# Kernel optimization log

Hardware: AMD Instinct MI355X
Metric: run time of the kernel (lower is better)

The kernel has to match this reference:

```python
import jax, jax.numpy as jnp
import numpy as np
from jax import lax

B, N, F_IN, F_OUT = 64, 256, 768, 256


def setup_inputs() -> dict:
    key = jax.random.key(0)
    ks = jax.random.split(key, 14)
    s = 0.02
    h = jax.random.normal(ks[0], (B, N, F_IN), jnp.float32)
    adj = jax.random.randint(ks[1], (B, N, N), 0, 2).astype(jnp.float32)
    return {
        'h': h,
        'adj': adj,
        'emb_W': jax.random.normal(ks[2], (F_OUT, F_IN), jnp.float32) * s,
        'ioux_W': jax.random.normal(ks[3], (2 * F_OUT, F_OUT), jnp.float32) * s,
        'ioux_b': jax.random.normal(ks[4], (2 * F_OUT,), jnp.float32) * s,
        'iouh_W': jax.random.normal(ks[5], (2 * F_OUT, F_OUT), jnp.float32) * s,
        'iouh_b': jax.random.normal(ks[6], (2 * F_OUT,), jnp.float32) * s,
        'coux_W': jax.random.normal(ks[7], (F_OUT, F_OUT), jnp.float32) * s,
        'coux_b': jax.random.normal(ks[8], (F_OUT,), jnp.float32) * s,
        'couh_W': jax.random.normal(ks[9], (F_OUT, F_OUT), jnp.float32) * s,
        'couh_b': jax.random.normal(ks[10], (F_OUT,), jnp.float32) * s,
        'fc_W': jax.random.normal(ks[11], (2, F_OUT), jnp.float32) * s,
        'fc_b': jax.random.normal(ks[12], (2,), jnp.float32) * s,
    }


def reference(h, adj, emb_W, ioux_W, ioux_b, iouh_W, iouh_b,
              coux_W, coux_b, couh_W, couh_b, fc_W, fc_b):
    # h: [B,N,F_IN], adj: [B,N,N]
    h_e = jnp.einsum('bnf,of->bno', h, emb_W)            # emb(h), no bias
    d = jnp.sum(adj, axis=-1)                            # row-degree [B,N]
    d_inv = jnp.where(d != 0, 1.0 / jnp.where(d != 0, d, 1.0), 0.0)
    # x-side projections depend only on the original h_e -> precompute once
    iou_x = jnp.einsum('bnf,of->bno', h_e, ioux_W) + ioux_b   # [B,N,2F]
    cou_x = jnp.einsum('bnf,of->bno', h_e, coux_W) + coux_b   # [B,N,F]

    n_nodes = h.shape[1]

    def step(h_copy, i):
        # Tree_Parent_AGG row i: p[b,i] = d_inv[b,i] * sum_j adj[b,j,i] * h_copy[b,j]
        adj_col = lax.dynamic_index_in_dim(adj, i, axis=2, keepdims=False)   # [B,N]
        dinv_i = lax.dynamic_index_in_dim(d_inv, i, axis=1, keepdims=False)  # [B]
        x_parent = jnp.einsum('bn,bnd->bd', adj_col, h_copy) * dinv_i[:, None]
        iou = lax.dynamic_index_in_dim(iou_x, i, axis=1, keepdims=False) \
              + x_parent @ iouh_W.T + iouh_b
        r, z = jnp.split(iou, 2, axis=1)
        r = jax.nn.sigmoid(r)
        z = jax.nn.sigmoid(z)
        hc = jnp.tanh(lax.dynamic_index_in_dim(cou_x, i, axis=1, keepdims=False)
                      + (r * x_parent) @ couh_W.T + couh_b)
        h_new = z * x_parent + (1.0 - z) * hc
        h_copy = lax.dynamic_update_index_in_dim(h_copy, h_new, i, axis=1)
        return h_copy, None

    h_final, _ = lax.scan(step, h_e, jnp.arange(n_nodes))
    pooled = jnp.max(h_final, axis=1)                    # [B,F]
    return pooled @ fc_W.T + fc_b                        # [B,2]
```

## Files before the change

kernel.cpp:

```cpp
#include <hip/hip_runtime.h>
#include <hip/hip_fp16.h>

#define NB    64
#define NN    256
#define FIN   768
#define FOUT  256

typedef _Float16 half8v __attribute__((ext_vector_type(8)));
typedef float    float4v __attribute__((ext_vector_type(4)));

__device__ inline unsigned char enc8(float v){
#if __has_builtin(__builtin_amdgcn_cvt_pk_fp8_f32)
  return (unsigned char)(__builtin_amdgcn_cvt_pk_fp8_f32(v, v, 0, false) & 0xFF);
#else
  float best = 1e30f; unsigned char bc = 0;
  for (int c = 0; c < 256; c++){
    if ((c & 0x7F) == 0x7F) continue;
    int e = (c >> 3) & 15, mnt = c & 7;
    float mag = e ? ldexpf(1.f + mnt*0.125f, e-7) : ldexpf(mnt*0.125f, -6);
    float d = (c >> 7) ? -mag : mag;
    float err = fabsf(v - d);
    if (err < best){ best = err; bc = (unsigned char)c; }
  }
  return bc;
#endif
}

__device__ inline float4v mfma_fp8(long long a, long long b, float4v c){
  return __builtin_amdgcn_mfma_f32_16x16x32_fp8_fp8(a, b, c, 0, 0, 0);
}
__device__ inline float4v mfma_f16(half8v a, half8v b, float4v c){
  return __builtin_amdgcn_mfma_f32_16x16x32_f16(a, b, c, 0, 0, 0);
}

#define RAW_BAR() do { \
    asm volatile("s_waitcnt lgkmcnt(0)" ::: "memory"); \
    __builtin_amdgcn_s_barrier(); \
  } while (0)

__global__ __launch_bounds__(256) void prep_kernel(
    const float* __restrict__ emb_W, const float* __restrict__ ioux_W,
    const float* __restrict__ ioux_b, const float* __restrict__ coux_W,
    const float* __restrict__ coux_b,
    _Float16* __restrict__ embW16, _Float16* __restrict__ Wcat16,
    float* __restrict__ biascat)
{
  int idx = blockIdx.x*256 + threadIdx.x;
  if (idx < 196608) { embW16[idx] = (_Float16)emb_W[idx]; return; }
  idx -= 196608;
  if (idx < 196608) {
    int o = idx >> 8, k = idx & 255;
    float v = (o < 512) ? ioux_W[o*256 + k] : coux_W[(o-512)*256 + k];
    Wcat16[idx] = (_Float16)v; return;
  }
  idx -= 196608;
  if (idx < 768) { biascat[idx] = (idx < 512) ? ioux_b[idx] : coux_b[idx-512]; return; }
}

__global__ __launch_bounds__(256) void quant_kernel(
    const float* __restrict__ iouh_W, const float* __restrict__ couh_W,
    unsigned char* __restrict__ iouh8, unsigned char* __restrict__ couh8,
    float* __restrict__ invrs_iou, float* __restrict__ invrs_cou)
{
  const int row = blockIdx.x;
  const int t   = threadIdx.x;
  const bool is_iou = (row < 512);
  const int rl = is_iou ? row : row - 512;
  const float w = is_iou ? iouh_W[(size_t)rl*256 + t] : couh_W[(size_t)rl*256 + t];

  __shared__ float sm[256];
  sm[t] = fabsf(w);
  __syncthreads();
  for (int s = 128; s > 0; s >>= 1){
    if (t < s) sm[t] = fmaxf(sm[t], sm[t+s]);
    __syncthreads();
  }
  const float mx = sm[0];
  const float rs = (mx > 1e-20f) ? (240.0f / mx) : 1.0f;
  const unsigned char byte = enc8(w * rs);
  const int off = ((rl>>4)*8 + (t>>5))*512 + ((t>>3)&3)*128 + (rl&15)*8 + (t&7);
  if (is_iou) iouh8[off] = byte; else couh8[off] = byte;
  if (t == 0){
    const float inv = 1.0f / (rs * 16.0f);
    if (is_iou) invrs_iou[rl] = inv; else invrs_cou[rl] = inv;
  }
}

__global__ __launch_bounds__(256) void degmask_kernel(
    const float* __restrict__ adj, unsigned int* __restrict__ maskw,
    float* __restrict__ dinv)
{
  const int b = blockIdx.x, t = threadIdx.x;
  __shared__ unsigned int rb[256][8];
  const float* rowp = adj + (size_t)b*NN*NN + (size_t)t*NN;
  float s = 0.f;
  #pragma unroll
  for (int qc = 0; qc < 8; qc++){
    unsigned int w = 0;
    const float4* rp = (const float4*)(rowp + qc*32);
    #pragma unroll
    for (int j4 = 0; j4 < 8; j4++){
      float4 v = rp[j4];
      s += v.x + v.y + v.z + v.w;
      const int sh = j4*4;
      w |= (v.x != 0.f ? 1u : 0u) << sh;
      w |= (v.y != 0.f ? 1u : 0u) << (sh+1);
      w |= (v.z != 0.f ? 1u : 0u) << (sh+2);
      w |= (v.w != 0.f ? 1u : 0u) << (sh+3);
    }
    rb[t][qc] = w;
  }
  dinv[b*NN + t] = (s != 0.f) ? 1.0f/s : 0.0f;
  __syncthreads();
  #pragma unroll
  for (int qc = 0; qc < 8; qc++){
    unsigned int w = 0;
    #pragma unroll
    for (int jj = 0; jj < 32; jj++)
      w |= ((rb[qc*32 + jj][t>>5] >> (t&31)) & 1u) << jj;
    maskw[((size_t)b*NN + t)*8 + qc] = w;
  }
}

template<int AF32>
__global__ __launch_bounds__(256) void gemm16_kernel(
    const void* __restrict__ Aq, const _Float16* __restrict__ Bw,
    _Float16* __restrict__ Cout, const float* __restrict__ bias,
    int M, int N, int K, int ldc)
{
  const int wave = threadIdx.x >> 6;
  const int lane = threadIdx.x & 63;
  const int m0 = (blockIdx.x*4 + wave)*16;
  const int n0 = blockIdx.y*64;
  const int mrow = m0 + (lane & 15);
  const int kgrp = lane >> 4;
  float4v acc[4];
  #pragma unroll
  for (int nt = 0; nt < 4; nt++) acc[nt] = (float4v){0.f,0.f,0.f,0.f};

  for (int k0 = 0; k0 < K; k0 += 32){
    const int ka = k0 + kgrp*8;
    half8v af;
    if (AF32){
      const float* A = (const float*)Aq;
      const float4* ap = (const float4*)(A + (size_t)mrow*K + ka);
      float4 a0 = ap[0], a1 = ap[1];
      af[0]=(_Float16)a0.x; af[1]=(_Float16)a0.y; af[2]=(_Float16)a0.z; af[3]=(_Float16)a0.w;
      af[4]=(_Float16)a1.x; af[5]=(_Float16)a1.y; af[6]=(_Float16)a1.z; af[7]=(_Float16)a1.w;
    } else {
      const _Float16* A = (const _Float16*)Aq;
      af = *(const half8v*)(A + (size_t)mrow*K + ka);
    }
    #pragma unroll
    for (int nt = 0; nt < 4; nt++){
      const int ncol = n0 + nt*16 + (lane & 15);
      half8v bf = *(const half8v*)(Bw + (size_t)ncol*K + ka);
      acc[nt] = __builtin_amdgcn_mfma_f32_16x16x32_f16(af, bf, acc[nt], 0, 0, 0);
    }
  }
  #pragma unroll
  for (int nt = 0; nt < 4; nt++){
    const int ncol = n0 + nt*16 + (lane & 15);
    const float bv = bias ? bias[ncol] : 0.f;
    #pragma unroll
    for (int r = 0; r < 4; r++){
      const int orow = m0 + (lane>>4)*4 + r;
      Cout[(size_t)orow*ldc + ncol] = (_Float16)(acc[nt][r] + bv);
    }
  }
}

__global__ __launch_bounds__(256) void transp_kernel(
    const _Float16* __restrict__ Hc, _Float16* __restrict__ HcT)
{
  const int b = blockIdx.x, fg = blockIdx.y;
  const int t = threadIdx.x;
  __shared__ _Float16 tile[32][264];
  #pragma unroll
  for (int pass = 0; pass < 4; pass++){
    const int n  = pass*64 + (t>>2);
    const int f8 = (t&3)*8;
    const half8v v = *(const half8v*)(Hc + (size_t)(b*NN + n)*FOUT + fg*32 + f8);
    #pragma unroll
    for (int e = 0; e < 8; e++) tile[f8+e][n] = v[e];
  }
  __syncthreads();
  const int f = t>>3, ch = t&7;
  _Float16* dst = HcT + ((size_t)b*FOUT + fg*32 + f)*NN + ch*32;
  #pragma unroll
  for (int k = 0; k < 4; k++)
    *(half8v*)(dst + k*8) = *(const half8v*)(&tile[f][ch*32 + k*8]);
}

#define OFF_BT   0
#define OFF_DT   33280
#define OFF_HNT  53760
#define OFF_XP32 74240
#define OFF_XP8  75264
#define OFF_P8   75520
#define OFF_Z    75776
#define OFF_PM   76800
#define OFF_MASK 77824
#define OFF_DINV 86016
#define SCAN_LDS 87040

__global__ __launch_bounds__(512, 2)
void scan_kernel(
    const _Float16* __restrict__ Hc,
    const _Float16* __restrict__ HcT,
    const _Float16* __restrict__ OUTX,
    const unsigned char* __restrict__ iouh8,
    const unsigned char* __restrict__ couh8,
    const float* __restrict__ invrs_iou,
    const float* __restrict__ invrs_cou,
    const float* __restrict__ dinv,
    const unsigned int* __restrict__ maskw,
    const float* __restrict__ iouh_b,
    const float* __restrict__ couh_b,
    const float* __restrict__ fc_W,
    const float* __restrict__ fc_b,
    float* __restrict__ out)
{
  const int b    = blockIdx.x;
  const int t    = threadIdx.x;
  const int wave = t >> 6;
  const int lane = t & 63;
  const int q    = lane >> 4;
  const int r    = lane & 15;
  const int f0   = 32*wave;

  extern __shared__ __align__(16) char smem[];
  float*         sh_xp32 = (float*)(smem + OFF_XP32);
  unsigned char* sh_xp8  = (unsigned char*)(smem + OFF_XP8);
  unsigned char* sh_p8   = (unsigned char*)(smem + OFF_P8);
  float*         sh_z    = (float*)(smem + OFF_Z);
  float*         sh_pm   = (float*)(smem + OFF_PM);
  unsigned int*  sh_mask = (unsigned int*)(smem + OFF_MASK);
  float*         sh_dinv = (float*)(smem + OFF_DINV);

  #pragma unroll
  for (int k = 0; k < 10; k++)
    ((unsigned int*)(smem + OFF_DT))[k*512 + t] = 0u;
  {
    const unsigned int* mg = maskw + ((size_t)b*NN)*8;
    #pragma unroll
    for (int k = 0; k < 4; k++) sh_mask[k*512 + t] = mg[k*512 + t];
    if (t < 256) sh_dinv[t] = dinv[(size_t)b*NN + t];
  }

  half8v Hreg[2][8];
  #pragma unroll
  for (int g = 0; g < 2; g++){
    const _Float16* hp = HcT + ((size_t)b*FOUT + f0 + 16*g + r)*NN + q*8;
    #pragma unroll
    for (int ks = 0; ks < 8; ks++)
      Hreg[g][ks] = *(const half8v*)(hp + ks*32);
  }

  long long ifrag[4][8];
  #pragma unroll
  for (int tt = 0; tt < 4; tt++)
    #pragma unroll
    for (int kc = 0; kc < 8; kc++)
      ifrag[tt][kc] = *(const long long*)(iouh8 + (size_t)(((4*wave+tt)*8 + kc)*512) + q*128 + r*8);
  long long cfrag[2][8];
  #pragma unroll
  for (int tt = 0; tt < 2; tt++)
    #pragma unroll
    for (int kc = 0; kc < 8; kc++)
      cfrag[tt][kc] = *(const long long*)(couh8 + (size_t)(((2*wave+tt)*8 + kc)*512) + q*128 + r*8);

  const int o1    = 64*wave + 16*(r>>2) + q*4 + (r&3);
  const int o_upd = 32*wave + 16*((r>>2)&1) + q*4 + (r&3);
  const float bi1 = iouh_b[o1];
  const float vi1 = invrs_iou[o1];
  const float bcou_l = couh_b[o_upd];
  const float invc_l = invrs_cou[o_upd];
  float pmax = -1e30f;

  _Float16 pf_oxi = OUTX[(size_t)b*NN*768 + o1];
  _Float16 pf_oxc = OUTX[(size_t)b*NN*768 + 512 + o_upd];
  _Float16 pf_he  = Hc[(size_t)b*NN*FOUT + o_upd];

  __syncthreads();
  unsigned int wl_cur = sh_mask[0];

  #pragma unroll 1
  for (int i = 0; i < NN; i++){

    if ((i & 31) == 0){
      const int tile = i >> 5;
      if (tile > 0){
        const int tprev = tile - 1;
        #pragma unroll
        for (int g = 0; g < 2; g++){
          const half8v hv = *(const half8v*)(smem + OFF_HNT + (f0 + 16*g + r)*80 + q*16);
          #pragma unroll
          for (int ks = 0; ks < 8; ks++) if (ks == tprev) Hreg[g][ks] = hv;
        }
      }
      float4v bacc[2][2];
      #pragma unroll
      for (int rt = 0; rt < 2; rt++)
        #pragma unroll
        for (int g = 0; g < 2; g++) bacc[rt][g] = (float4v){0.f,0.f,0.f,0.f};
      #pragma unroll
      for (int rt = 0; rt < 2; rt++){
        #pragma unroll
        for (int ks = 0; ks < 8; ks++){
          const unsigned int wm = sh_mask[(i + rt*16 + r)*8 + ks];
          half8v am;
          #pragma unroll
          for (int e = 0; e < 8; e++)
            am[e] = (_Float16)((wm >> (q*8 + e)) & 1u);
          bacc[rt][0] = mfma_f16(am, Hreg[0][ks], bacc[rt][0]);
          bacc[rt][1] = mfma_f16(am, Hreg[1][ks], bacc[rt][1]);
        }
      }
      #pragma unroll
      for (int rt = 0; rt < 2; rt++)
        #pragma unroll
        for (int g = 0; g < 2; g++)
          #pragma unroll
          for (int jj = 0; jj < 4; jj++)
            *(float*)(smem + (rt*16 + q*4 + jj)*1040 + (f0 + 16*g + r)*4) = bacc[rt][g][jj];
    }

    const int li = i & 31;
    const unsigned int wl_next = sh_mask[((i+1)&255)*8 + (((i+1)>>5)&7)];

    const float oxi = (float)pf_oxi;
    const float oxc = (float)pf_oxc;
    const float he  = (float)pf_he;
    {
      const size_t rown = (size_t)b*NN + ((i+1) & 255);
      pf_oxi = OUTX[rown*768 + o1];
      pf_oxc = OUTX[rown*768 + 512 + o_upd];
      pf_he  = Hc[rown*FOUT + o_upd];
    }
    const float dv = sh_dinv[i];

    {
      const unsigned int wl = wl_cur & ((1u << li) - 1u);
      half8v af;
      #pragma unroll
      for (int e = 0; e < 8; e++)
        af[e] = (_Float16)((wl >> (q*8 + e)) & 1u);
      #pragma unroll
      for (int g = 0; g < 2; g++){
        const int fg = f0 + 16*g + r;
        const half8v bf = *(const half8v*)(smem + OFF_DT + fg*80 + q*16);
        float4v ag = (float4v){0.f,0.f,0.f,0.f};
        ag = mfma_f16(af, bf, ag);
        const float bt = *(const float*)(smem + li*1040 + fg*4);
        const float xp = (bt + ag[0]) * dv;
        if (q == 0)      sh_xp32[fg] = xp;
        else if (q == 1) sh_xp8[fg] = enc8(xp * 16.f);
      }
    }
    wl_cur = wl_next;
    RAW_BAR();

    {
      float4v iacc[4];
      #pragma unroll
      for (int tt = 0; tt < 4; tt++) iacc[tt] = (float4v){0.f,0.f,0.f,0.f};
      #pragma unroll
      for (int kc = 0; kc < 8; kc++){
        const long long bfr = *(const long long*)(sh_xp8 + kc*32 + q*8);
        #pragma unroll
        for (int tt = 0; tt < 4; tt++)
          iacc[tt] = mfma_fp8(ifrag[tt][kc], bfr, iacc[tt]);
      }
      float d1 = 0.f;
      #pragma unroll
      for (int tt = 0; tt < 4; tt++) if ((r>>2) == tt){
        #pragma unroll
        for (int jj = 0; jj < 4; jj++) if ((r&3) == jj) d1 = iacc[tt][jj];
      }
      const float g1 = d1*vi1 + oxi + bi1;
      const float sg = 1.f / (1.f + __expf(-g1));
      if (wave < 4) sh_p8[o1] = enc8(sg * sh_xp32[o1] * 16.f);
      else          sh_z[o1 - 256] = sg;
    }
    RAW_BAR();

    {
      float4v cacc[2];
      cacc[0] = (float4v){0.f,0.f,0.f,0.f};
      cacc[1] = cacc[0];
      #pragma unroll
      for (int kc = 0; kc < 8; kc++){
        const long long bfr = *(const long long*)(sh_p8 + kc*32 + q*8);
        cacc[0] = mfma_fp8(cfrag[0][kc], bfr, cacc[0]);
        cacc[1] = mfma_fp8(cfrag[1][kc], bfr, cacc[1]);
      }
      if (r < 8){
        float cd = 0.f;
        #pragma unroll
        for (int tt = 0; tt < 2; tt++) if ((r>>2) == tt){
          #pragma unroll
          for (int jj = 0; jj < 4; jj++) if ((r&3) == jj) cd = cacc[tt][jj];
        }
        const float v   = cd*invc_l + oxc + bcou_l;
        const float hcv = tanhf(v);
        const float z   = sh_z[o_upd];
        const float xpv = sh_xp32[o_upd];
        const float hn  = z*xpv + (1.f - z)*hcv;
        pmax = fmaxf(pmax, hn);
        *(_Float16*)(smem + OFF_DT  + o_upd*80 + li*2) = (_Float16)(hn - he);
        *(_Float16*)(smem + OFF_HNT + o_upd*80 + li*2) = (_Float16)hn;
      }
    }
  }

  if (r < 8) sh_pm[o_upd] = pmax;
  __syncthreads();
  if (t < 128){
    const int c = t >> 6;
    float s = 0.f;
    #pragma unroll
    for (int qq = 0; qq < 4; qq++){
      const int f = (t & 63) + qq*64;
      s += fc_W[c*256 + f] * sh_pm[f];
    }
    #pragma unroll
    for (int off = 32; off > 0; off >>= 1) s += __shfl_xor(s, off, 64);
    if ((t & 63) == 0) out[b*2 + c] = s + fc_b[c];
  }
}

extern "C" void kernel_launch(void* const* d_in, const int* in_sizes, int n_in,
                              void* d_out, int out_size, void* d_ws, size_t ws_size,
                              hipStream_t stream)
{
  (void)in_sizes; (void)n_in; (void)out_size; (void)ws_size;
  const float* h      = (const float*)d_in[0];
  const float* adj    = (const float*)d_in[1];
  const float* emb_W  = (const float*)d_in[2];
  const float* ioux_W = (const float*)d_in[3];
  const float* ioux_b = (const float*)d_in[4];
  const float* iouh_W = (const float*)d_in[5];
  const float* iouh_b = (const float*)d_in[6];
  const float* coux_W = (const float*)d_in[7];
  const float* coux_b = (const float*)d_in[8];
  const float* couh_W = (const float*)d_in[9];
  const float* couh_b = (const float*)d_in[10];
  const float* fc_W   = (const float*)d_in[11];
  const float* fc_b   = (const float*)d_in[12];
  float* out = (float*)d_out;

  size_t off = 0;
  char* base = (char*)d_ws;
  auto carve = [&](size_t bytes)->char* {
    off = (off + 255) & ~(size_t)255;
    char* p = base + off;
    off += bytes;
    return p;
  };
  _Float16* embW16 = (_Float16*)carve((size_t)256*768*2);
  _Float16* Wcat16 = (_Float16*)carve((size_t)768*256*2);
  float*    biascat= (float*)  carve((size_t)768*4);
  unsigned char* iouh8 = (unsigned char*)carve(131072);
  unsigned char* couh8 = (unsigned char*)carve(65536);
  float*    invrs_iou = (float*)carve(512*4);
  float*    invrs_cou = (float*)carve(256*4);
  float*    dinv   = (float*)  carve((size_t)NB*NN*4);
  unsigned int* maskw = (unsigned int*)carve((size_t)NB*NN*8*4 + 64);
  _Float16* Hc     = (_Float16*)carve((size_t)NB*NN*FOUT*2);
  _Float16* HcT    = (_Float16*)carve((size_t)NB*NN*FOUT*2);
  _Float16* OUTX   = (_Float16*)carve((size_t)NB*NN*768*2);

  hipFuncSetAttribute((const void*)scan_kernel,
                      hipFuncAttributeMaxDynamicSharedMemorySize, SCAN_LDS);

  prep_kernel<<<dim3(1539), dim3(256), 0, stream>>>(
      emb_W, ioux_W, ioux_b, coux_W, coux_b, embW16, Wcat16, biascat);

  quant_kernel<<<dim3(768), dim3(256), 0, stream>>>(
      iouh_W, couh_W, iouh8, couh8, invrs_iou, invrs_cou);

  degmask_kernel<<<dim3(NB), dim3(256), 0, stream>>>(adj, maskw, dinv);

  gemm16_kernel<1><<<dim3(256, 4), dim3(256), 0, stream>>>(
      (const void*)h, embW16, Hc, nullptr, NB*NN, FOUT, FIN, FOUT);

  transp_kernel<<<dim3(NB, 8), dim3(256), 0, stream>>>(Hc, HcT);

  gemm16_kernel<0><<<dim3(256, 12), dim3(256), 0, stream>>>(
      (const void*)Hc, Wcat16, OUTX, biascat, NB*NN, 768, FOUT, 768);

  scan_kernel<<<dim3(NB), dim3(512), SCAN_LDS, stream>>>(
      Hc, HcT, OUTX, iouh8, couh8, invrs_iou, invrs_cou, dinv, maskw,
      iouh_b, couh_b, fc_W, fc_b, out);
}
```

Baseline: 654.8 us.

## Precompute next-step intra-tile parent correction during gate matmul and split MFMA chains

The per-step intra-tile parent aggregation MFMA for the next node is moved into the iou-gate phase, so it overlaps the fp8 gate MFMAs instead of sitting on the critical path before the first barrier. At step start only the newest row's delta is added as a scalar correction. The gate and candidate fp8 MFMA accumulations are split into two independent chains to shorten dependency latency. The separate fp16 copy of h_new in LDS is removed and Hreg is rebuilt by adding the stored deltas, which cuts LDS use and writes but changes rounding (fp16 delta accumulation).

```diff
diff --git a/kernel.cpp b/kernel.cpp
--- a/kernel.cpp
+++ b/kernel.cpp
@@ -194,15 +194,14 @@
 
 #define OFF_BT   0
 #define OFF_DT   33280
-#define OFF_HNT  53760
-#define OFF_XP32 74240
-#define OFF_XP8  75264
-#define OFF_P8   75520
-#define OFF_Z    75776
-#define OFF_PM   76800
-#define OFF_MASK 77824
-#define OFF_DINV 86016
-#define SCAN_LDS 87040
+#define OFF_XP32 53760
+#define OFF_XP8  54784
+#define OFF_P8   55040
+#define OFF_Z    55296
+#define OFF_PM   56320
+#define OFF_MASK 57344
+#define OFF_DINV 65536
+#define SCAN_LDS 66560
 
 __global__ __launch_bounds__(512, 2)
 void scan_kernel(
@@ -285,18 +284,22 @@
   __syncthreads();
   unsigned int wl_cur = sh_mask[0];
 
+  float cp[2]  = {0.f, 0.f};
+  float btn[2] = {0.f, 0.f};
+
   #pragma unroll 1
   for (int i = 0; i < NN; i++){
-
-    if ((i & 31) == 0){
+    const int li = i & 31;
+
+    if (li == 0){
       const int tile = i >> 5;
       if (tile > 0){
         const int tprev = tile - 1;
         #pragma unroll
         for (int g = 0; g < 2; g++){
-          const half8v hv = *(const half8v*)(smem + OFF_HNT + (f0 + 16*g + r)*80 + q*16);
+          const half8v dvv = *(const half8v*)(smem + OFF_DT + (f0 + 16*g + r)*80 + q*16);
           #pragma unroll
-          for (int ks = 0; ks < 8; ks++) if (ks == tprev) Hreg[g][ks] = hv;
+          for (int ks = 0; ks < 8; ks++) if (ks == tprev) Hreg[g][ks] = Hreg[g][ks] + dvv;
         }
       }
       float4v bacc[2][2];
@@ -324,9 +327,13 @@
           #pragma unroll
           for (int jj = 0; jj < 4; jj++)
             *(float*)(smem + (rt*16 + q*4 + jj)*1040 + (f0 + 16*g + r)*4) = bacc[rt][g][jj];
-    }
-
-    const int li = i & 31;
+      #pragma unroll
+      for (int g = 0; g < 2; g++){
+        btn[g] = *(const float*)(smem +  (f0 + 16*g + r)*4);
+        cp[g] = 0.f;
+      }
+    }
+
     const unsigned int wl_next = sh_mask[((i+1)&255)*8 + (((i+1)>>5)&7)];
 
     const float oxi = (float)pf_oxi;
@@ -341,42 +348,60 @@
     const float dv = sh_dinv[i];
 
     {
-      const unsigned int wl = wl_cur & ((1u << li) - 1u);
-      half8v af;
-      #pragma unroll
-      for (int e = 0; e < 8; e++)
-        af[e] = (_Float16)((wl >> (q*8 + e)) & 1u);
       #pragma unroll
       for (int g = 0; g < 2; g++){
         const int fg = f0 + 16*g + r;
-        const half8v bf = *(const half8v*)(smem + OFF_DT + fg*80 + q*16);
-        float4v ag = (float4v){0.f,0.f,0.f,0.f};
-        ag = mfma_f16(af, bf, ag);
-        const float bt = *(const float*)(smem + li*1040 + fg*4);
-        const float xp = (bt + ag[0]) * dv;
+        float corr = cp[g];
+        if (li > 0 && ((wl_cur >> (li-1)) & 1u))
+          corr += (float)*(const _Float16*)(smem + OFF_DT + fg*80 + (li-1)*2);
+        const float xp = (btn[g] + corr) * dv;
         if (q == 0)      sh_xp32[fg] = xp;
         else if (q == 1) sh_xp8[fg] = enc8(xp * 16.f);
       }
     }
-    wl_cur = wl_next;
     RAW_BAR();
 
+    float xpv_pre = 0.f;
     {
-      float4v iacc[4];
-      #pragma unroll
-      for (int tt = 0; tt < 4; tt++) iacc[tt] = (float4v){0.f,0.f,0.f,0.f};
-      #pragma unroll
-      for (int kc = 0; kc < 8; kc++){
-        const long long bfr = *(const long long*)(sh_xp8 + kc*32 + q*8);
-        #pragma unroll
-        for (int tt = 0; tt < 4; tt++)
-          iacc[tt] = mfma_fp8(ifrag[tt][kc], bfr, iacc[tt]);
-      }
+      float4v iacc[4][2];
+      #pragma unroll
+      for (int tt = 0; tt < 4; tt++){
+        iacc[tt][0] = (float4v){0.f,0.f,0.f,0.f};
+        iacc[tt][1] = iacc[tt][0];
+      }
+      #pragma unroll
+      for (int kc = 0; kc < 4; kc++){
+        const long long blo = *(const long long*)(sh_xp8 + kc*32 + q*8);
+        const long long bhi = *(const long long*)(sh_xp8 + (kc+4)*32 + q*8);
+        #pragma unroll
+        for (int tt = 0; tt < 4; tt++){
+          iacc[tt][0] = mfma_fp8(ifrag[tt][kc],   blo, iacc[tt][0]);
+          iacc[tt][1] = mfma_fp8(ifrag[tt][kc+4], bhi, iacc[tt][1]);
+        }
+      }
+      if (li < 31){
+        const unsigned int wl = wl_next & ((1u << li) - 1u);
+        half8v af;
+        #pragma unroll
+        for (int e = 0; e < 8; e++)
+          af[e] = (_Float16)((wl >> (q*8 + e)) & 1u);
+        #pragma unroll
+        for (int g = 0; g < 2; g++){
+          const int fg = f0 + 16*g + r;
+          const half8v bf = *(const half8v*)(smem + OFF_DT + fg*80 + q*16);
+          float4v ag = (float4v){0.f,0.f,0.f,0.f};
+          ag = mfma_f16(af, bf, ag);
+          cp[g] = ag[0];
+          btn[g] = *(const float*)(smem + (li+1)*1040 + fg*4);
+        }
+      }
+      xpv_pre = sh_xp32[o_upd];
       float d1 = 0.f;
       #pragma unroll
       for (int tt = 0; tt < 4; tt++) if ((r>>2) == tt){
         #pragma unroll
-        for (int jj = 0; jj < 4; jj++) if ((r&3) == jj) d1 = iacc[tt][jj];
+        for (int jj = 0; jj < 4; jj++) if ((r&3) == jj)
+          d1 = iacc[tt][0][jj] + iacc[tt][1][jj];
       }
       const float g1 = d1*vi1 + oxi + bi1;
       const float sg = 1.f / (1.f + __expf(-g1));
@@ -386,32 +411,39 @@
     RAW_BAR();
 
     {
-      float4v cacc[2];
-      cacc[0] = (float4v){0.f,0.f,0.f,0.f};
-      cacc[1] = cacc[0];
-      #pragma unroll
-      for (int kc = 0; kc < 8; kc++){
-        const long long bfr = *(const long long*)(sh_p8 + kc*32 + q*8);
-        cacc[0] = mfma_fp8(cfrag[0][kc], bfr, cacc[0]);
-        cacc[1] = mfma_fp8(cfrag[1][kc], bfr, cacc[1]);
+      float4v cacc[2][2];
+      #pragma unroll
+      for (int tt = 0; tt < 2; tt++){
+        cacc[tt][0] = (float4v){0.f,0.f,0.f,0.f};
+        cacc[tt][1] = cacc[tt][0];
+      }
+      #pragma unroll
+      for (int kc = 0; kc < 4; kc++){
+        const long long blo = *(const long long*)(sh_p8 + kc*32 + q*8);
+        const long long bhi = *(const long long*)(sh_p8 + (kc+4)*32 + q*8);
+        #pragma unroll
+        for (int tt = 0; tt < 2; tt++){
+          cacc[tt][0] = mfma_fp8(cfrag[tt][kc],   blo, cacc[tt][0]);
+          cacc[tt][1] = mfma_fp8(cfrag[tt][kc+4], bhi, cacc[tt][1]);
+        }
       }
       if (r < 8){
         float cd = 0.f;
         #pragma unroll
         for (int tt = 0; tt < 2; tt++) if ((r>>2) == tt){
           #pragma unroll
-          for (int jj = 0; jj < 4; jj++) if ((r&3) == jj) cd = cacc[tt][jj];
+          for (int jj = 0; jj < 4; jj++) if ((r&3) == jj)
+            cd = cacc[tt][0][jj] + cacc[tt][1][jj];
         }
         const float v   = cd*invc_l + oxc + bcou_l;
         const float hcv = tanhf(v);
         const float z   = sh_z[o_upd];
-        const float xpv = sh_xp32[o_upd];
-        const float hn  = z*xpv + (1.f - z)*hcv;
+        const float hn  = z*xpv_pre + (1.f - z)*hcv;
         pmax = fmaxf(pmax, hn);
-        *(_Float16*)(smem + OFF_DT  + o_upd*80 + li*2) = (_Float16)(hn - he);
-        *(_Float16*)(smem + OFF_HNT + o_upd*80 + li*2) = (_Float16)hn;
-      }
-    }
+        *(_Float16*)(smem + OFF_DT + o_upd*80 + li*2) = (_Float16)(hn - he);
+      }
+    }
+    wl_cur = wl_next;
   }
 
   if (r < 8) sh_pm[o_upd] = pmax;
```

Result: slower. 749.6 us (+14.5%).
